# Optimization experiments

Measured on AMD Instinct MI355X. Metric: run time of the kernel, lower is better.

## Reference

```python
import jax, jax.numpy as jnp
import numpy as np

COMMITMENT_COST = 0.25
EPS = 1e-10


def setup_inputs() -> dict:
    key = jax.random.key(0)
    k1, k2 = jax.random.split(key)
    x = jax.random.normal(k1, (64, 4096, 64), dtype=jnp.float32)          # [B, T, D]
    embedding = jax.random.normal(k2, (512, 64), dtype=jnp.float32)       # [K, D] codebook
    return {"x": x, "embedding": embedding}


def reference(x, embedding):
    B, T, D = x.shape
    K = embedding.shape[0]
    flat = x.reshape(-1, D)                                               # [N, D]
    N = flat.shape[0]

    distances = (jnp.sum(flat * flat, axis=1, keepdims=True)
                 - 2.0 * (flat @ embedding.T)
                 + jnp.sum(embedding * embedding, axis=1))

    idx = jnp.argmin(distances, axis=1)                                   # [N] nearest code
    quantized = embedding[idx].reshape(x.shape)                           # gather lookup

    # commitment loss (EMA variant: only e_latent_loss, codebook frozen w.r.t. loss)
    e_latent_loss = jnp.mean((jax.lax.stop_gradient(quantized) - x) ** 2)
    loss = COMMITMENT_COST * e_latent_loss

    # straight-through estimator
    q_st = x + jax.lax.stop_gradient(quantized - x)

    # perplexity via scatter-add histogram of code usage
    counts = jnp.zeros((K,), dtype=x.dtype).at[idx].add(jnp.ones((), x.dtype))
    avg_probs = counts / jnp.asarray(N, x.dtype)
    perplexity = jnp.exp(-jnp.sum(avg_probs * jnp.log(avg_probs + EPS)))

    return q_st, loss, perplexity
```

## Files before the change

### kernel.cpp

```cpp
#include <hip/hip_runtime.h>
#include <math.h>

#define N_ROWS   262144
#define DIM      64
#define KCODES   512
#define MT       64
#define NTHREADS 256
#define NBLOCKS  (N_ROWS / MT)
#define XS_STRIDE 68
#define ES_STRIDE 72
#define CHUNK    64
#define NCHUNK   (KCODES / CHUNK)
#define MARGIN   2e-3f

typedef float f32x4 __attribute__((ext_vector_type(4)));
typedef short s16x8 __attribute__((ext_vector_type(8)));


__device__ __forceinline__ unsigned short f2bf(float f) {
    unsigned u = __float_as_uint(f);
    unsigned r = u + 0x7fffu + ((u >> 16) & 1u);
    return (unsigned short)(r >> 16);
}
__device__ __forceinline__ float bf2f(unsigned short h) {
    return __uint_as_float(((unsigned)h) << 16);
}

__global__ __launch_bounds__(64) void vq_prep(const float* __restrict__ emb,
                                              float* __restrict__ esq,
                                              int* __restrict__ counts,
                                              float* __restrict__ lossAdj,
                                              unsigned short* __restrict__ eh,
                                              unsigned short* __restrict__ el) {
    int k = blockIdx.x * 64 + threadIdx.x;
    const float* e = emb + (size_t)k * DIM;
    float s = 0.f;
    #pragma unroll
    for (int d = 0; d < DIM; ++d) s += e[d] * e[d];
    esq[k] = s;
    counts[k] = 0;
    #pragma unroll
    for (int d = 0; d < DIM; ++d) {
        float v = e[d];
        unsigned short h = f2bf(v);
        eh[k * DIM + d] = h;
        el[k * DIM + d] = f2bf(v - bf2f(h));
    }
    if (k == 0) *lossAdj = 0.f;
}

__global__ __launch_bounds__(NTHREADS, 4) void vq_main(
    const float* __restrict__ x, const float* __restrict__ emb,
    const float* __restrict__ g_esq,
    const unsigned short* __restrict__ eh_g, const unsigned short* __restrict__ el_g,
    unsigned short* __restrict__ g_idx, float* __restrict__ g_lossPart,
    float* __restrict__ lossAdj, float* __restrict__ out)
{
    __shared__ float xs[MT * XS_STRIDE];
    __shared__ unsigned short ehs[CHUNK * ES_STRIDE];
    __shared__ unsigned short els[CHUNK * ES_STRIDE];
    __shared__ float esq_s[KCODES];
    __shared__ int   idx_s[MT];
    __shared__ int   flg_s[MT];
    __shared__ int   flist[MT];
    __shared__ int   nflag;
    __shared__ float wred[4];

    const int tid  = threadIdx.x;
    const int R0   = blockIdx.x * MT;
    const int w    = tid >> 6;
    const int lane = tid & 63;
    const int m    = lane & 15;
    const int q    = lane >> 4;

    #pragma unroll
    for (int i = 0; i < 4; ++i) {
        int flat = tid + NTHREADS * i;
        int r  = flat >> 4;
        int qc = flat & 15;
        f32x4 v = *(const f32x4*)&x[(size_t)(R0 + r) * DIM + 4 * qc];
        *(f32x4*)&xs[r * XS_STRIDE + 4 * qc] = v;
    }
    esq_s[tid]       = g_esq[tid];
    esq_s[tid + 256] = g_esq[tid + 256];
    if (tid == 0) nflag = 0;
    __syncthreads();

    s16x8 axh[2], axl[2];
    const int lrow = w * 16 + m;
    #pragma unroll
    for (int kc = 0; kc < 2; ++kc) {
        f32x4 xv0 = *(const f32x4*)&xs[lrow * XS_STRIDE + kc * 32 + q * 8];
        f32x4 xv1 = *(const f32x4*)&xs[lrow * XS_STRIDE + kc * 32 + q * 8 + 4];
        s16x8 h, l;
        #pragma unroll
        for (int t = 0; t < 8; ++t) {
            float v = (t < 4) ? xv0[t] : xv1[t - 4];
            unsigned short hb = f2bf(v);
            h[t] = (short)hb;
            l[t] = (short)f2bf(v - bf2f(hb));
        }
        axh[kc] = h; axl[kc] = l;
    }

    float b1[4], b2[4]; int i1[4];
    #pragma unroll
    for (int r = 0; r < 4; ++r) { b1[r] = 3.4e38f; b2[r] = 3.4e38f; i1[r] = 0; }

    for (int c = 0; c < NCHUNK; ++c) {
        if (c) __syncthreads();
        #pragma unroll
        for (int i = 0; i < 2; ++i) {
            int ch = tid + NTHREADS * i;
            int rl = ch >> 3, off = (ch & 7) * 8;
            size_t gofs = (size_t)(c * CHUNK + rl) * DIM + off;
            *(s16x8*)&ehs[rl * ES_STRIDE + off] = *(const s16x8*)&eh_g[gofs];
            *(s16x8*)&els[rl * ES_STRIDE + off] = *(const s16x8*)&el_g[gofs];
        }
        __syncthreads();

        f32x4 acc[4];
        #pragma unroll
        for (int ct = 0; ct < 4; ++ct) acc[ct] = (f32x4){0.f, 0.f, 0.f, 0.f};
        #pragma unroll
        for (int ct = 0; ct < 4; ++ct) {
            #pragma unroll
            for (int kc = 0; kc < 2; ++kc) {
                const int bofs = (ct * 16 + m) * ES_STRIDE + kc * 32 + q * 8;
                s16x8 bh = *(const s16x8*)&ehs[bofs];
                s16x8 bl = *(const s16x8*)&els[bofs];
                acc[ct] = __builtin_amdgcn_mfma_f32_16x16x32_bf16(axh[kc], bh, acc[ct], 0, 0, 0);
                acc[ct] = __builtin_amdgcn_mfma_f32_16x16x32_bf16(axl[kc], bh, acc[ct], 0, 0, 0);
                acc[ct] = __builtin_amdgcn_mfma_f32_16x16x32_bf16(axh[kc], bl, acc[ct], 0, 0, 0);
            }
        }
        #pragma unroll
        for (int ct = 0; ct < 4; ++ct) {
            int col = c * CHUNK + ct * 16 + m;
            float e2 = esq_s[col];
            #pragma unroll
            for (int r = 0; r < 4; ++r) {
                float dist = e2 - 2.f * acc[ct][r];
                if (dist < b1[r]) { b2[r] = b1[r]; b1[r] = dist; i1[r] = col; }
                else if (dist < b2[r]) b2[r] = dist;
            }
        }
    }

    #pragma unroll
    for (int s = 1; s < 16; s <<= 1) {
        #pragma unroll
        for (int r = 0; r < 4; ++r) {
            float ob1 = __shfl_xor(b1[r], s);
            int   oi1 = __shfl_xor(i1[r], s);
            float ob2 = __shfl_xor(b2[r], s);
            bool owin = (ob1 < b1[r]) || (ob1 == b1[r] && oi1 < i1[r]);
            float lb1 = owin ? b1[r] : ob1;
            b2[r] = fminf(fminf(b2[r], ob2), lb1);
            if (owin) { b1[r] = ob1; i1[r] = oi1; }
        }
    }
    if (m == 0) {
        #pragma unroll
        for (int r = 0; r < 4; ++r) {
            int lrw = w * 16 + q * 4 + r;
            idx_s[lrw] = i1[r];
            flg_s[lrw] = (b2[r] - b1[r] < MARGIN) ? 1 : 0;
        }
    }
    __syncthreads();

    if (tid < MT) {
        if (flg_s[tid]) { int p = atomicAdd(&nflag, 1); flist[p] = tid; }
        else g_idx[R0 + tid] = (unsigned short)idx_s[tid];
    }

    const int r  = tid >> 2;
    const int d0 = (tid & 3) * 16;
    float lpart = 0.f;
    if (!flg_s[r]) {
        const int ki = idx_s[r];
        const float* erow = emb + (size_t)ki * DIM;
        #pragma unroll
        for (int s4 = 0; s4 < 4; ++s4) {
            int d = d0 + 4 * s4;
            f32x4 e4 = *(const f32x4*)&erow[d];
            f32x4 xv = *(const f32x4*)&xs[r * XS_STRIDE + d];
            float f0 = e4.x - xv.x, f1 = e4.y - xv.y, f2 = e4.z - xv.z, f3 = e4.w - xv.w;
            f32x4 o = {xv.x + f0, xv.y + f1, xv.z + f2, xv.w + f3};
            *(f32x4*)&out[(size_t)(R0 + r) * DIM + d] = o;
            lpart += f0*f0 + f1*f1 + f2*f2 + f3*f3;
        }
    }
    #pragma unroll
    for (int off = 32; off > 0; off >>= 1) lpart += __shfl_down(lpart, off);
    if ((tid & 63) == 0) wred[tid >> 6] = lpart;
    __syncthreads();
    if (tid == 0) g_lossPart[blockIdx.x] = wred[0] + wred[1] + wred[2] + wred[3];

    for (int fi = w; fi < nflag; fi += 4) {
        int row = R0 + flist[fi];
        const float* xr = &x[(size_t)row * DIM];
        float best = 3.4e38f; int bidx = 0;
        #pragma unroll
        for (int j = 0; j < 8; ++j) {
            int cc = lane * 8 + j;
            const float* er = &emb[(size_t)cc * DIM];
            float dot = 0.f;
            #pragma unroll
            for (int d = 0; d < DIM; ++d) dot = fmaf(xr[d], er[d], dot);
            float dist = g_esq[cc] - 2.f * dot;
            if (dist < best) { best = dist; bidx = cc; }
        }
        #pragma unroll
        for (int s = 1; s < 64; s <<= 1) {
            float ob = __shfl_xor(best, s);
            int   oi = __shfl_xor(bidx, s);
            if (ob < best || (ob == best && oi < bidx)) { best = ob; bidx = oi; }
        }
        float xv = xr[lane];
        float ev = emb[(size_t)bidx * DIM + lane];
        float f  = ev - xv;
        out[(size_t)row * DIM + lane] = xv + f;
        float lp = f * f;
        #pragma unroll
        for (int s = 1; s < 64; s <<= 1) lp += __shfl_xor(lp, s);
        if (lane == 0) {
            atomicAdd(lossAdj, lp);
            g_idx[row] = (unsigned short)bidx;
        }
    }
}

__global__ __launch_bounds__(256) void vq_hist(const unsigned short* __restrict__ g_idx,
                                               int* __restrict__ counts) {
    __shared__ int h[KCODES];
    int t = threadIdx.x;
    h[t] = 0; h[t + 256] = 0;
    __syncthreads();
    const unsigned short* p = g_idx + (size_t)blockIdx.x * 4096;
    #pragma unroll
    for (int i = 0; i < 16; ++i)
        atomicAdd(&h[p[t + 256 * i]], 1);
    __syncthreads();
    int v0 = h[t], v1 = h[t + 256];
    if (v0) atomicAdd(&counts[t], v0);
    if (v1) atomicAdd(&counts[t + 256], v1);
}

__global__ __launch_bounds__(512) void vq_final(const int* __restrict__ counts,
                                                const float* __restrict__ lossPart,
                                                const float* __restrict__ lossAdj,
                                                float* __restrict__ out) {
    __shared__ float redp[8];
    __shared__ float redl[8];
    int k = threadIdx.x;
    float p = (float)counts[k] * (1.f / 262144.f);
    float t = p * logf(p + 1e-10f);
    float l = 0.f;
    #pragma unroll
    for (int i = 0; i < 8; ++i) l += lossPart[k + 512 * i];
    #pragma unroll
    for (int off = 32; off > 0; off >>= 1) {
        t += __shfl_down(t, off);
        l += __shfl_down(l, off);
    }
    if ((k & 63) == 0) { redp[k >> 6] = t; redl[k >> 6] = l; }
    __syncthreads();
    if (k == 0) {
        float s = 0.f, ls = 0.f;
        #pragma unroll
        for (int i = 0; i < 8; ++i) { s += redp[i]; ls += redl[i]; }
        out[16777216] = (ls + *lossAdj) * (0.25f / 16777216.f);
        out[16777217] = expf(-s);
    }
}

extern "C" void kernel_launch(void* const* d_in, const int* in_sizes, int n_in,
                              void* d_out, int out_size, void* d_ws, size_t ws_size,
                              hipStream_t stream) {
    const float* x   = (const float*)d_in[0];
    const float* emb = (const float*)d_in[1];
    float* out = (float*)d_out;

    char* ws = (char*)d_ws;
    float*          esq      = (float*)(ws + 0);
    int*            counts   = (int*)(ws + 2048);
    float*          lossAdj  = (float*)(ws + 4096);
    unsigned short* eh       = (unsigned short*)(ws + 4608);
    unsigned short* el       = (unsigned short*)(ws + 70144);
    unsigned short* gidx     = (unsigned short*)(ws + 168448);
    float*          lossPart = (float*)(ws + 692736);

    vq_prep<<<8, 64, 0, stream>>>(emb, esq, counts, lossAdj, eh, el);
    vq_main<<<NBLOCKS, NTHREADS, 0, stream>>>(x, emb, esq, eh, el,
                                              gidx, lossPart, lossAdj, out);
    vq_hist<<<64, 256, 0, stream>>>(gidx, counts);
    vq_final<<<1, 512, 0, stream>>>(counts, lossPart, lossAdj, out);
}
```

Baseline: 292.6 us.

## Fuse histogram into main kernel, drop x LDS staging, widen codebook chunks

Removes the separate histogram kernel by having each block atomically add its 64 final indices into global counts after the fallback pass. It also stops staging x in shared memory and reads x rows straight from global memory. The codebook chunk size doubles to 128 with fewer barriers, the occupancy hint drops from 4 to 3, the top-2 tracking becomes branchless min/max, and the prep kernel writes vectorised bf16 stores. The costs are heavy global atomic contention on 512 counters across 4096 blocks, repeated global reads of x, and more register and LDS pressure per block.

```diff
diff --git a/kernel.cpp b/kernel.cpp
--- a/kernel.cpp
+++ b/kernel.cpp
@@ -7,9 +7,8 @@
 #define MT       64
 #define NTHREADS 256
 #define NBLOCKS  (N_ROWS / MT)
-#define XS_STRIDE 68
 #define ES_STRIDE 72
-#define CHUNK    64
+#define CHUNK    128
 #define NCHUNK   (KCODES / CHUNK)
 #define MARGIN   2e-3f
 
@@ -40,23 +39,28 @@
     esq[k] = s;
     counts[k] = 0;
     #pragma unroll
-    for (int d = 0; d < DIM; ++d) {
-        float v = e[d];
-        unsigned short h = f2bf(v);
-        eh[k * DIM + d] = h;
-        el[k * DIM + d] = f2bf(v - bf2f(h));
+    for (int c8 = 0; c8 < 8; ++c8) {
+        s16x8 h8, l8;
+        #pragma unroll
+        for (int j = 0; j < 8; ++j) {
+            float v = e[c8 * 8 + j];
+            unsigned short hb = f2bf(v);
+            h8[j] = (short)hb;
+            l8[j] = (short)f2bf(v - bf2f(hb));
+        }
+        *(s16x8*)&eh[k * DIM + c8 * 8] = h8;
+        *(s16x8*)&el[k * DIM + c8 * 8] = l8;
     }
     if (k == 0) *lossAdj = 0.f;
 }
 
-__global__ __launch_bounds__(NTHREADS, 4) void vq_main(
+__global__ __launch_bounds__(NTHREADS, 3) void vq_main(
     const float* __restrict__ x, const float* __restrict__ emb,
     const float* __restrict__ g_esq,
     const unsigned short* __restrict__ eh_g, const unsigned short* __restrict__ el_g,
     unsigned short* __restrict__ g_idx, float* __restrict__ g_lossPart,
-    float* __restrict__ lossAdj, float* __restrict__ out)
+    float* __restrict__ lossAdj, int* __restrict__ counts, float* __restrict__ out)
 {
-    __shared__ float xs[MT * XS_STRIDE];
     __shared__ unsigned short ehs[CHUNK * ES_STRIDE];
     __shared__ unsigned short els[CHUNK * ES_STRIDE];
     __shared__ float esq_s[KCODES];
@@ -73,25 +77,17 @@
     const int m    = lane & 15;
     const int q    = lane >> 4;
 
-    #pragma unroll
-    for (int i = 0; i < 4; ++i) {
-        int flat = tid + NTHREADS * i;
-        int r  = flat >> 4;
-        int qc = flat & 15;
-        f32x4 v = *(const f32x4*)&x[(size_t)(R0 + r) * DIM + 4 * qc];
-        *(f32x4*)&xs[r * XS_STRIDE + 4 * qc] = v;
-    }
     esq_s[tid]       = g_esq[tid];
     esq_s[tid + 256] = g_esq[tid + 256];
     if (tid == 0) nflag = 0;
-    __syncthreads();
 
     s16x8 axh[2], axl[2];
     const int lrow = w * 16 + m;
+    const float* xrow = x + (size_t)(R0 + lrow) * DIM;
     #pragma unroll
     for (int kc = 0; kc < 2; ++kc) {
-        f32x4 xv0 = *(const f32x4*)&xs[lrow * XS_STRIDE + kc * 32 + q * 8];
-        f32x4 xv1 = *(const f32x4*)&xs[lrow * XS_STRIDE + kc * 32 + q * 8 + 4];
+        f32x4 xv0 = *(const f32x4*)&xrow[kc * 32 + q * 8];
+        f32x4 xv1 = *(const f32x4*)&xrow[kc * 32 + q * 8 + 4];
         s16x8 h, l;
         #pragma unroll
         for (int t = 0; t < 8; ++t) {
@@ -110,7 +106,7 @@
     for (int c = 0; c < NCHUNK; ++c) {
         if (c) __syncthreads();
         #pragma unroll
-        for (int i = 0; i < 2; ++i) {
+        for (int i = 0; i < 4; ++i) {
             int ch = tid + NTHREADS * i;
             int rl = ch >> 3, off = (ch & 7) * 8;
             size_t gofs = (size_t)(c * CHUNK + rl) * DIM + off;
@@ -119,11 +115,11 @@
         }
         __syncthreads();
 
-        f32x4 acc[4];
-        #pragma unroll
-        for (int ct = 0; ct < 4; ++ct) acc[ct] = (f32x4){0.f, 0.f, 0.f, 0.f};
-        #pragma unroll
-        for (int ct = 0; ct < 4; ++ct) {
+        f32x4 acc[8];
+        #pragma unroll
+        for (int ct = 0; ct < 8; ++ct) acc[ct] = (f32x4){0.f, 0.f, 0.f, 0.f};
+        #pragma unroll
+        for (int ct = 0; ct < 8; ++ct) {
             #pragma unroll
             for (int kc = 0; kc < 2; ++kc) {
                 const int bofs = (ct * 16 + m) * ES_STRIDE + kc * 32 + q * 8;
@@ -135,14 +131,16 @@
             }
         }
         #pragma unroll
-        for (int ct = 0; ct < 4; ++ct) {
+        for (int ct = 0; ct < 8; ++ct) {
             int col = c * CHUNK + ct * 16 + m;
             float e2 = esq_s[col];
             #pragma unroll
             for (int r = 0; r < 4; ++r) {
                 float dist = e2 - 2.f * acc[ct][r];
-                if (dist < b1[r]) { b2[r] = b1[r]; b1[r] = dist; i1[r] = col; }
-                else if (dist < b2[r]) b2[r] = dist;
+                bool win = dist < b1[r];
+                b2[r] = fminf(fmaxf(dist, b1[r]), b2[r]);
+                b1[r] = fminf(b1[r], dist);
+                i1[r] = win ? col : i1[r];
             }
         }
     }
@@ -181,11 +179,12 @@
     if (!flg_s[r]) {
         const int ki = idx_s[r];
         const float* erow = emb + (size_t)ki * DIM;
+        const float* xr   = x + (size_t)(R0 + r) * DIM;
         #pragma unroll
         for (int s4 = 0; s4 < 4; ++s4) {
             int d = d0 + 4 * s4;
             f32x4 e4 = *(const f32x4*)&erow[d];
-            f32x4 xv = *(const f32x4*)&xs[r * XS_STRIDE + d];
+            f32x4 xv = *(const f32x4*)&xr[d];
             float f0 = e4.x - xv.x, f1 = e4.y - xv.y, f2 = e4.z - xv.z, f3 = e4.w - xv.w;
             f32x4 o = {xv.x + f0, xv.y + f1, xv.z + f2, xv.w + f3};
             *(f32x4*)&out[(size_t)(R0 + r) * DIM + d] = o;
@@ -199,7 +198,8 @@
     if (tid == 0) g_lossPart[blockIdx.x] = wred[0] + wred[1] + wred[2] + wred[3];
 
     for (int fi = w; fi < nflag; fi += 4) {
-        int row = R0 + flist[fi];
+        int lrw = flist[fi];
+        int row = R0 + lrw;
         const float* xr = &x[(size_t)row * DIM];
         float best = 3.4e38f; int bidx = 0;
         #pragma unroll
@@ -228,24 +228,12 @@
         if (lane == 0) {
             atomicAdd(lossAdj, lp);
             g_idx[row] = (unsigned short)bidx;
-        }
-    }
-}
-
-__global__ __launch_bounds__(256) void vq_hist(const unsigned short* __restrict__ g_idx,
-                                               int* __restrict__ counts) {
-    __shared__ int h[KCODES];
-    int t = threadIdx.x;
-    h[t] = 0; h[t + 256] = 0;
-    __syncthreads();
-    const unsigned short* p = g_idx + (size_t)blockIdx.x * 4096;
-    #pragma unroll
-    for (int i = 0; i < 16; ++i)
-        atomicAdd(&h[p[t + 256 * i]], 1);
-    __syncthreads();
-    int v0 = h[t], v1 = h[t + 256];
-    if (v0) atomicAdd(&counts[t], v0);
-    if (v1) atomicAdd(&counts[t + 256], v1);
+            idx_s[lrw] = bidx;
+        }
+    }
+    __syncthreads();
+
+    if (tid < MT) atomicAdd(&counts[idx_s[tid]], 1);
 }
 
 __global__ __launch_bounds__(512) void vq_final(const int* __restrict__ counts,
@@ -294,7 +282,6 @@
 
     vq_prep<<<8, 64, 0, stream>>>(emb, esq, counts, lossAdj, eh, el);
     vq_main<<<NBLOCKS, NTHREADS, 0, stream>>>(x, emb, esq, eh, el,
-                                              gidx, lossPart, lossAdj, out);
-    vq_hist<<<64, 256, 0, stream>>>(gidx, counts);
+                                              gidx, lossPart, lossAdj, counts, out);
     vq_final<<<1, 512, 0, stream>>>(counts, lossPart, lossAdj, out);
 }
```

New measurement: 332.1 us. 1.14x slower.
